# Performance work log

Hardware: AMD Instinct MI355X
Metric: run time of the kernel (lower is better)

## Reference

```python
import jax, jax.numpy as jnp
import numpy as np

T, B, I, H = 512, 64, 512, 512

def setup_inputs() -> dict:
    key = jax.random.key(0)
    k1, k2, k3 = jax.random.split(key, 3)
    # scale weights to keep tanh out of deep saturation
    return {
        "input": jax.random.normal(k1, (T, B, I), dtype=jnp.float32),
        "w_ih": jax.random.normal(k2, (H, I), dtype=jnp.float32) / np.sqrt(I),
        "w_hh": jax.random.normal(k3, (H, H), dtype=jnp.float32) / np.sqrt(H),
    }

def reference(input, w_ih, w_hh):
    # vanilla tanh RNN: h_t = tanh(x_t @ w_ih^T + h_{t-1} @ w_hh^T)
    batch = input.shape[1]
    h0 = jnp.zeros((batch, w_hh.shape[0]), dtype=input.dtype)

    def step(h_prev, x):
        h = jnp.tanh(x @ w_ih.T + h_prev @ w_hh.T)
        return h, h

    h_last, h_all = jax.lax.scan(step, h0, input)
    return h_all, h_last
```

## Files before the change

### kernel.cpp

```cpp
#include <hip/hip_runtime.h>
#include <cmath>

#define T_STEPS 512
#define BATCH   64
#define ISZ     512
#define HSZ     512
#define EXN     32768

__device__ __forceinline__ void ex_store(unsigned long long* w, float h, unsigned tag) {
    union { float f; unsigned u; } c; c.f = h;
    const unsigned long long v = ((unsigned long long)tag << 32) | (unsigned long long)c.u;
    __hip_atomic_store(w, v, __ATOMIC_RELAXED, __HIP_MEMORY_SCOPE_AGENT);
}

__device__ __forceinline__ float4 ld_pin_f4(const float* p) {
    float4 v;
    asm volatile("global_load_dwordx4 %0, %1, off" : "=v"(v) : "v"(p));
    return v;
}

__device__ __forceinline__ float dot16_fold(const float4 (&W)[4][4],
                                            const float4* __restrict__ src,
                                            int parbase4, int kseg) {
    const float4* s0 = src + parbase4 + kseg * 5;
    const float4* s1 = s0 + 160;
    float A0 = 0.f, A1 = 0.f, A2 = 0.f, A3 = 0.f;
    float B0 = 0.f, B1 = 0.f, B2 = 0.f, B3 = 0.f;
    #pragma unroll
    for (int i = 0; i < 4; ++i) {
        const float4 h0 = s0[i];
        const float4 h1 = s1[i];
        const float4 w0 = W[0][i], w1 = W[1][i], w2 = W[2][i], w3 = W[3][i];
        A0 = fmaf(w0.x, h0.x, A0); A0 = fmaf(w0.y, h0.y, A0);
        A0 = fmaf(w0.z, h0.z, A0); A0 = fmaf(w0.w, h0.w, A0);
        A1 = fmaf(w1.x, h0.x, A1); A1 = fmaf(w1.y, h0.y, A1);
        A1 = fmaf(w1.z, h0.z, A1); A1 = fmaf(w1.w, h0.w, A1);
        A2 = fmaf(w2.x, h0.x, A2); A2 = fmaf(w2.y, h0.y, A2);
        A2 = fmaf(w2.z, h0.z, A2); A2 = fmaf(w2.w, h0.w, A2);
        A3 = fmaf(w3.x, h0.x, A3); A3 = fmaf(w3.y, h0.y, A3);
        A3 = fmaf(w3.z, h0.z, A3); A3 = fmaf(w3.w, h0.w, A3);
        B0 = fmaf(w0.x, h1.x, B0); B0 = fmaf(w0.y, h1.y, B0);
        B0 = fmaf(w0.z, h1.z, B0); B0 = fmaf(w0.w, h1.w, B0);
        B1 = fmaf(w1.x, h1.x, B1); B1 = fmaf(w1.y, h1.y, B1);
        B1 = fmaf(w1.z, h1.z, B1); B1 = fmaf(w1.w, h1.w, B1);
        B2 = fmaf(w2.x, h1.x, B2); B2 = fmaf(w2.y, h1.y, B2);
        B2 = fmaf(w2.z, h1.z, B2); B2 = fmaf(w2.w, h1.w, B2);
        B3 = fmaf(w3.x, h1.x, B3); B3 = fmaf(w3.y, h1.y, B3);
        B3 = fmaf(w3.z, h1.z, B3); B3 = fmaf(w3.w, h1.w, B3);
    }
    const bool sb0 = (kseg & 1) != 0;
    const bool sb1 = (kseg & 2) != 0;
    const bool sb2 = (kseg & 4) != 0;
    const float u0 = (sb0 ? B0 : A0) + __shfl_xor(sb0 ? A0 : B0, 1, 64);
    const float u1 = (sb0 ? B1 : A1) + __shfl_xor(sb0 ? A1 : B1, 1, 64);
    const float u2 = (sb0 ? B2 : A2) + __shfl_xor(sb0 ? A2 : B2, 1, 64);
    const float u3 = (sb0 ? B3 : A3) + __shfl_xor(sb0 ? A3 : B3, 1, 64);
    const float w01 = (sb1 ? u1 : u0) + __shfl_xor(sb1 ? u0 : u1, 2, 64);
    const float w23 = (sb1 ? u3 : u2) + __shfl_xor(sb1 ? u2 : u3, 2, 64);
    float z = (sb2 ? w23 : w01) + __shfl_xor(sb2 ? w01 : w23, 4, 64);
    z += __shfl_xor(z, 8, 64);
    z += __shfl_xor(z, 16, 64);
    return z;
}

__global__ __launch_bounds__(512, 2) void rnn_fused(const float* __restrict__ x,
                                                    const float* __restrict__ wih,
                                                    const float* __restrict__ whh,
                                                    float* __restrict__ out,
                                                    unsigned long long* __restrict__ ex) {
    __shared__ __align__(16) float hls[2560];
    __shared__ __align__(16) float xss[2560];
    const float4* hl4 = (const float4*)hls;
    const float4* xs4 = (const float4*)xss;

    const int tid  = threadIdx.x;
    const int bid  = blockIdx.x;
    const int xcd  = bid & 7;
    const int ib   = bid >> 3;
    const int p    = xcd * 4 + (ib & 3);
    const int g    = ib >> 2;
    const int kseg = tid & 31;
    const int jg   = tid >> 5;
    const int jb   = g * 64 + jg * 4;

    float4 wh[4][4], wi[4][4];
    #pragma unroll
    for (int r = 0; r < 4; ++r) {
        const float* hr = whh + (size_t)(jb + r) * HSZ + kseg * 16;
        const float* ir = wih + (size_t)(jb + r) * ISZ + kseg * 16;
        #pragma unroll
        for (int i = 0; i < 4; ++i) {
            wh[r][i] = ld_pin_f4(hr + 4 * i);
            wi[r][i] = ld_pin_f4(ir + 4 * i);
        }
    }
    asm volatile("s_waitcnt vmcnt(0)" ::: "memory");
    __builtin_amdgcn_sched_barrier(0);

    unsigned long long* exw0 = ex + (size_t)(2 * p + 0) * 512 + tid;
    unsigned long long* exw1 = ex + (size_t)(2 * p + 1) * 512 + tid;

    const int whf = (tid >> 4) * 20 + ((tid >> 2) & 3) * 4 + (tid & 3);

    const int bx = tid >> 8;
    const int io = (tid & 255) * 2;
    const int xf = bx * 640 + (io >> 4) * 20 + ((io >> 2) & 3) * 4 + (io & 3);
    const float* xsrc = x + (size_t)(2 * p + bx) * ISZ + io;

    const int row  = ((kseg >> 1) & 1) + 2 * ((kseg >> 2) & 1);
    const int br   = kseg & 1;
    const int outj = jb + row;
    const int outb = 2 * p + br;
    float* outp = out + (size_t)outb * HSZ + outj;
    unsigned long long* exself = ex + (size_t)outb * 512 + outj;

    {
        const float2 v = *(const float2*)xsrc;
        *(float2*)&xss[xf] = v;
    }
    __syncthreads();
    float xwv = dot16_fold(wi, xs4, 0, kseg);

    for (int t = 0; t < T_STEPS; ++t) {
        const int  parh4 = (t & 1) * 320;
        const bool havex = (t < T_STEPS - 1);

        float2 xv;
        if (havex) xv = *(const float2*)(xsrc + (size_t)(t + 1) * (BATCH * ISZ));

        if (t > 0) {
            const size_t soff = (size_t)((t - 1) & 1) * EXN;
            unsigned long long v0 = __hip_atomic_load(exw0 + soff, __ATOMIC_RELAXED,
                                                      __HIP_MEMORY_SCOPE_AGENT);
            unsigned long long v1 = __hip_atomic_load(exw1 + soff, __ATOMIC_RELAXED,
                                                      __HIP_MEMORY_SCOPE_AGENT);
            while ((unsigned)(v0 >> 32) != (unsigned)t ||
                   (unsigned)(v1 >> 32) != (unsigned)t) {
                __builtin_amdgcn_s_sleep(1);
                v0 = __hip_atomic_load(exw0 + soff, __ATOMIC_RELAXED,
                                       __HIP_MEMORY_SCOPE_AGENT);
                v1 = __hip_atomic_load(exw1 + soff, __ATOMIC_RELAXED,
                                       __HIP_MEMORY_SCOPE_AGENT);
            }
            union { unsigned u; float f; } c0, c1;
            c0.u = (unsigned)v0; c1.u = (unsigned)v1;
            hls[parh4 * 4 + whf]       = c0.f;
            hls[parh4 * 4 + 640 + whf] = c1.f;
        }
        if (havex) *(float2*)&xss[((t + 1) & 1) * 1280 + xf] = xv;
        __syncthreads();

        float acc = 0.f;
        if (t > 0)
            acc = dot16_fold(wh, hl4, parh4, kseg);

        if (kseg < 8) {
            const float a2 = acc + xwv;
            const float e  = __expf(2.f * a2);
            const float hv = 1.f - 2.f / (e + 1.f);
            outp[(size_t)t * (BATCH * HSZ)] = hv;
            if (havex)
                ex_store(exself + (size_t)(t & 1) * EXN, hv, (unsigned)(t + 1));
            else
                out[(size_t)T_STEPS * BATCH * HSZ + (size_t)outb * HSZ + outj] = hv;
        }

        if (havex)
            xwv = dot16_fold(wi, xs4, ((t + 1) & 1) * 320, kseg);
    }
}

extern "C" void kernel_launch(void* const* d_in, const int* in_sizes, int n_in,
                              void* d_out, int out_size, void* d_ws, size_t ws_size,
                              hipStream_t stream) {
    (void)in_sizes; (void)n_in; (void)out_size; (void)ws_size;
    const float* x   = (const float*)d_in[0];
    const float* wih = (const float*)d_in[1];
    const float* whh = (const float*)d_in[2];
    float*       out = (float*)d_out;
    unsigned long long* ex = (unsigned long long*)d_ws;

    (void)hipMemsetAsync(d_ws, 0, 2 * EXN * sizeof(unsigned long long), stream);

    hipLaunchKernelGGL(rnn_fused, dim3(256), dim3(512), 0, stream,
                       x, wih, whh, out, ex);
}
```

Baseline: 1.020 ms.

## Split batch work into two pipelined halves with 2-row weight tiles per thread

Each block now owns 4 batch rows and 32 hidden units instead of 2 batch rows and 64 units, with each thread holding 2 weight rows rather than 4, which halves register-resident weights. Each timestep is split into two phases. The block waits on the exchange flags for the first batch pair, computes and publishes those results, then waits on the second pair. This lets other blocks' dependencies on the first pair resolve earlier and shortens the per-thread dot product, at the cost of an extra __syncthreads, more flag polling per step, and single-buffered LDS reuse that relies on the barrier ordering.

After: 1.916 ms. 87.7% more time.

```diff
diff --git a/kernel.cpp b/kernel.cpp
--- a/kernel.cpp
+++ b/kernel.cpp
@@ -19,45 +19,32 @@
     return v;
 }
 
-__device__ __forceinline__ float dot16_fold(const float4 (&W)[4][4],
-                                            const float4* __restrict__ src,
-                                            int parbase4, int kseg) {
-    const float4* s0 = src + parbase4 + kseg * 5;
+__device__ __forceinline__ float dot2_fold(const float4 (&W)[2][4],
+                                           const float4* __restrict__ src,
+                                           int base4, int kseg) {
+    const float4* s0 = src + base4 + kseg * 5;
     const float4* s1 = s0 + 160;
-    float A0 = 0.f, A1 = 0.f, A2 = 0.f, A3 = 0.f;
-    float B0 = 0.f, B1 = 0.f, B2 = 0.f, B3 = 0.f;
+    float A0 = 0.f, A1 = 0.f, B0 = 0.f, B1 = 0.f;
     #pragma unroll
     for (int i = 0; i < 4; ++i) {
         const float4 h0 = s0[i];
         const float4 h1 = s1[i];
-        const float4 w0 = W[0][i], w1 = W[1][i], w2 = W[2][i], w3 = W[3][i];
+        const float4 w0 = W[0][i], w1 = W[1][i];
         A0 = fmaf(w0.x, h0.x, A0); A0 = fmaf(w0.y, h0.y, A0);
         A0 = fmaf(w0.z, h0.z, A0); A0 = fmaf(w0.w, h0.w, A0);
         A1 = fmaf(w1.x, h0.x, A1); A1 = fmaf(w1.y, h0.y, A1);
         A1 = fmaf(w1.z, h0.z, A1); A1 = fmaf(w1.w, h0.w, A1);
-        A2 = fmaf(w2.x, h0.x, A2); A2 = fmaf(w2.y, h0.y, A2);
-        A2 = fmaf(w2.z, h0.z, A2); A2 = fmaf(w2.w, h0.w, A2);
-        A3 = fmaf(w3.x, h0.x, A3); A3 = fmaf(w3.y, h0.y, A3);
-        A3 = fmaf(w3.z, h0.z, A3); A3 = fmaf(w3.w, h0.w, A3);
         B0 = fmaf(w0.x, h1.x, B0); B0 = fmaf(w0.y, h1.y, B0);
         B0 = fmaf(w0.z, h1.z, B0); B0 = fmaf(w0.w, h1.w, B0);
         B1 = fmaf(w1.x, h1.x, B1); B1 = fmaf(w1.y, h1.y, B1);
         B1 = fmaf(w1.z, h1.z, B1); B1 = fmaf(w1.w, h1.w, B1);
-        B2 = fmaf(w2.x, h1.x, B2); B2 = fmaf(w2.y, h1.y, B2);
-        B2 = fmaf(w2.z, h1.z, B2); B2 = fmaf(w2.w, h1.w, B2);
-        B3 = fmaf(w3.x, h1.x, B3); B3 = fmaf(w3.y, h1.y, B3);
-        B3 = fmaf(w3.z, h1.z, B3); B3 = fmaf(w3.w, h1.w, B3);
     }
     const bool sb0 = (kseg & 1) != 0;
     const bool sb1 = (kseg & 2) != 0;
-    const bool sb2 = (kseg & 4) != 0;
     const float u0 = (sb0 ? B0 : A0) + __shfl_xor(sb0 ? A0 : B0, 1, 64);
     const float u1 = (sb0 ? B1 : A1) + __shfl_xor(sb0 ? A1 : B1, 1, 64);
-    const float u2 = (sb0 ? B2 : A2) + __shfl_xor(sb0 ? A2 : B2, 1, 64);
-    const float u3 = (sb0 ? B3 : A3) + __shfl_xor(sb0 ? A3 : B3, 1, 64);
-    const float w01 = (sb1 ? u1 : u0) + __shfl_xor(sb1 ? u0 : u1, 2, 64);
-    const float w23 = (sb1 ? u3 : u2) + __shfl_xor(sb1 ? u2 : u3, 2, 64);
-    float z = (sb2 ? w23 : w01) + __shfl_xor(sb2 ? w01 : w23, 4, 64);
+    float z = (sb1 ? u1 : u0) + __shfl_xor(sb1 ? u0 : u1, 2, 64);
+    z += __shfl_xor(z, 4, 64);
     z += __shfl_xor(z, 8, 64);
     z += __shfl_xor(z, 16, 64);
     return z;
@@ -77,15 +64,16 @@
     const int bid  = blockIdx.x;
     const int xcd  = bid & 7;
     const int ib   = bid >> 3;
-    const int p    = xcd * 4 + (ib & 3);
-    const int g    = ib >> 2;
+    const int pg   = xcd * 2 + (ib & 1);
+    const int g    = ib >> 1;
     const int kseg = tid & 31;
     const int jg   = tid >> 5;
-    const int jb   = g * 64 + jg * 4;
-
-    float4 wh[4][4], wi[4][4];
+    const int jb   = g * 32 + jg * 2;
+    const int b0   = pg * 4;
+
+    float4 wh[2][4], wi[2][4];
     #pragma unroll
-    for (int r = 0; r < 4; ++r) {
+    for (int r = 0; r < 2; ++r) {
         const float* hr = whh + (size_t)(jb + r) * HSZ + kseg * 16;
         const float* ir = wih + (size_t)(jb + r) * ISZ + kseg * 16;
         #pragma unroll
@@ -97,76 +85,116 @@
     asm volatile("s_waitcnt vmcnt(0)" ::: "memory");
     __builtin_amdgcn_sched_barrier(0);
 
-    unsigned long long* exw0 = ex + (size_t)(2 * p + 0) * 512 + tid;
-    unsigned long long* exw1 = ex + (size_t)(2 * p + 1) * 512 + tid;
+    unsigned long long* exw00 = ex + (size_t)(b0 + 0) * 512 + tid;
+    unsigned long long* exw01 = ex + (size_t)(b0 + 1) * 512 + tid;
+    unsigned long long* exw10 = ex + (size_t)(b0 + 2) * 512 + tid;
+    unsigned long long* exw11 = ex + (size_t)(b0 + 3) * 512 + tid;
 
     const int whf = (tid >> 4) * 20 + ((tid >> 2) & 3) * 4 + (tid & 3);
 
-    const int bx = tid >> 8;
-    const int io = (tid & 255) * 2;
-    const int xf = bx * 640 + (io >> 4) * 20 + ((io >> 2) & 3) * 4 + (io & 3);
-    const float* xsrc = x + (size_t)(2 * p + bx) * ISZ + io;
-
-    const int row  = ((kseg >> 1) & 1) + 2 * ((kseg >> 2) & 1);
-    const int br   = kseg & 1;
+    const int bx  = tid >> 7;
+    const int idx = tid & 127;
+    const int xf4 = bx * 160 + (idx >> 2) * 5 + (idx & 3);
+    const float* xsrc = x + (size_t)(b0 + bx) * ISZ + idx * 4;
+
+    const int bsel = kseg & 1;
+    const int row  = (kseg >> 1) & 1;
     const int outj = jb + row;
-    const int outb = 2 * p + br;
-    float* outp = out + (size_t)outb * HSZ + outj;
-    unsigned long long* exself = ex + (size_t)outb * 512 + outj;
-
-    {
-        const float2 v = *(const float2*)xsrc;
-        *(float2*)&xss[xf] = v;
-    }
+    const int ob0  = b0 + bsel;
+    const int ob1  = b0 + 2 + bsel;
+    float* outp0 = out + (size_t)ob0 * HSZ + outj;
+    float* outp1 = out + (size_t)ob1 * HSZ + outj;
+    unsigned long long* exs0 = ex + (size_t)ob0 * 512 + outj;
+    unsigned long long* exs1 = ex + (size_t)ob1 * 512 + outj;
+
+    ((float4*)xss)[xf4] = *(const float4*)xsrc;
     __syncthreads();
-    float xwv = dot16_fold(wi, xs4, 0, kseg);
+    float xw0 = dot2_fold(wi, xs4, 0,   kseg);
+    float xw1 = dot2_fold(wi, xs4, 320, kseg);
 
     for (int t = 0; t < T_STEPS; ++t) {
-        const int  parh4 = (t & 1) * 320;
         const bool havex = (t < T_STEPS - 1);
 
-        float2 xv;
-        if (havex) xv = *(const float2*)(xsrc + (size_t)(t + 1) * (BATCH * ISZ));
+        float4 xv;
+        if (havex) xv = *(const float4*)(xsrc + (size_t)(t + 1) * (BATCH * ISZ));
+
+        const size_t soff = (size_t)((t - 1) & 1) * EXN;
 
         if (t > 0) {
-            const size_t soff = (size_t)((t - 1) & 1) * EXN;
-            unsigned long long v0 = __hip_atomic_load(exw0 + soff, __ATOMIC_RELAXED,
-                                                      __HIP_MEMORY_SCOPE_AGENT);
-            unsigned long long v1 = __hip_atomic_load(exw1 + soff, __ATOMIC_RELAXED,
+            unsigned long long v0 = __hip_atomic_load(exw00 + soff, __ATOMIC_RELAXED,
+                                                      __HIP_MEMORY_SCOPE_AGENT);
+            unsigned long long v1 = __hip_atomic_load(exw01 + soff, __ATOMIC_RELAXED,
                                                       __HIP_MEMORY_SCOPE_AGENT);
             while ((unsigned)(v0 >> 32) != (unsigned)t ||
                    (unsigned)(v1 >> 32) != (unsigned)t) {
                 __builtin_amdgcn_s_sleep(1);
-                v0 = __hip_atomic_load(exw0 + soff, __ATOMIC_RELAXED,
-                                       __HIP_MEMORY_SCOPE_AGENT);
-                v1 = __hip_atomic_load(exw1 + soff, __ATOMIC_RELAXED,
+                v0 = __hip_atomic_load(exw00 + soff, __ATOMIC_RELAXED,
+                                       __HIP_MEMORY_SCOPE_AGENT);
+                v1 = __hip_atomic_load(exw01 + soff, __ATOMIC_RELAXED,
                                        __HIP_MEMORY_SCOPE_AGENT);
             }
             union { unsigned u; float f; } c0, c1;
             c0.u = (unsigned)v0; c1.u = (unsigned)v1;
-            hls[parh4 * 4 + whf]       = c0.f;
-            hls[parh4 * 4 + 640 + whf] = c1.f;
-        }
-        if (havex) *(float2*)&xss[((t + 1) & 1) * 1280 + xf] = xv;
+            hls[whf]       = c0.f;
+            hls[640 + whf] = c1.f;
+        }
         __syncthreads();
 
-        float acc = 0.f;
-        if (t > 0)
-            acc = dot16_fold(wh, hl4, parh4, kseg);
-
-        if (kseg < 8) {
-            const float a2 = acc + xwv;
-            const float e  = __expf(2.f * a2);
-            const float hv = 1.f - 2.f / (e + 1.f);
-            outp[(size_t)t * (BATCH * HSZ)] = hv;
-            if (havex)
-                ex_store(exself + (size_t)(t & 1) * EXN, hv, (unsigned)(t + 1));
-            else
-                out[(size_t)T_STEPS * BATCH * HSZ + (size_t)outb * HSZ + outj] = hv;
-        }
-
-        if (havex)
-            xwv = dot16_fold(wi, xs4, ((t + 1) & 1) * 320, kseg);
+        {
+            float acc = 0.f;
+            if (t > 0) acc = dot2_fold(wh, hl4, 0, kseg);
+            if (kseg < 4) {
+                const float a2 = acc + xw0;
+                const float e  = __expf(2.f * a2);
+                const float hv = 1.f - 2.f / (e + 1.f);
+                outp0[(size_t)t * (BATCH * HSZ)] = hv;
+                if (havex)
+                    ex_store(exs0 + (size_t)(t & 1) * EXN, hv, (unsigned)(t + 1));
+                else
+                    out[(size_t)T_STEPS * BATCH * HSZ + (size_t)ob0 * HSZ + outj] = hv;
+            }
+        }
+
+        if (t > 0) {
+            unsigned long long v0 = __hip_atomic_load(exw10 + soff, __ATOMIC_RELAXED,
+                                                      __HIP_MEMORY_SCOPE_AGENT);
+            unsigned long long v1 = __hip_atomic_load(exw11 + soff, __ATOMIC_RELAXED,
+                                                      __HIP_MEMORY_SCOPE_AGENT);
+            while ((unsigned)(v0 >> 32) != (unsigned)t ||
+                   (unsigned)(v1 >> 32) != (unsigned)t) {
+                __builtin_amdgcn_s_sleep(1);
+                v0 = __hip_atomic_load(exw10 + soff, __ATOMIC_RELAXED,
+                                       __HIP_MEMORY_SCOPE_AGENT);
+                v1 = __hip_atomic_load(exw11 + soff, __ATOMIC_RELAXED,
+                                       __HIP_MEMORY_SCOPE_AGENT);
+            }
+            union { unsigned u; float f; } c0, c1;
+            c0.u = (unsigned)v0; c1.u = (unsigned)v1;
+            hls[1280 + whf] = c0.f;
+            hls[1920 + whf] = c1.f;
+        }
+        if (havex) ((float4*)xss)[xf4] = xv;
+        __syncthreads();
+
+        {
+            float acc = 0.f;
+            if (t > 0) acc = dot2_fold(wh, hl4, 320, kseg);
+            if (kseg < 4) {
+                const float a2 = acc + xw1;
+                const float e  = __expf(2.f * a2);
+                const float hv = 1.f - 2.f / (e + 1.f);
+                outp1[(size_t)t * (BATCH * HSZ)] = hv;
+                if (havex)
+                    ex_store(exs1 + (size_t)(t & 1) * EXN, hv, (unsigned)(t + 1));
+                else
+                    out[(size_t)T_STEPS * BATCH * HSZ + (size_t)ob1 * HSZ + outj] = hv;
+            }
+        }
+
+        if (havex) {
+            xw0 = dot2_fold(wi, xs4, 0,   kseg);
+            xw1 = dot2_fold(wi, xs4, 320, kseg);
+        }
     }
 }
 
```

## Split RNN into input-projection phase then recurrence with one batch per block

Applied to the files above, without the earlier changes.

The kernel now first computes x_t·W_ih^T for all timesteps into the output buffer, with no cross-block sync. It then reloads W_hh into the same registers and runs the recurrence, reading the precomputed projection back. Each block now handles one batch row and 8 output rows per thread group instead of two batch rows and 4 rows. This halves the weight registers per thread and removes the input dot product from the serial critical path. The cost is a full extra write and read of a T×B×H intermediate through global memory, and each block still has to poll the exchange buffer every step.

New measurement: 1.165 ms. 1.14x slower.

```diff
diff --git a/kernel.cpp b/kernel.cpp
--- a/kernel.cpp
+++ b/kernel.cpp
@@ -19,45 +19,42 @@
     return v;
 }
 
-__device__ __forceinline__ float dot16_fold(const float4 (&W)[4][4],
-                                            const float4* __restrict__ src,
-                                            int parbase4, int kseg) {
-    const float4* s0 = src + parbase4 + kseg * 5;
-    const float4* s1 = s0 + 160;
-    float A0 = 0.f, A1 = 0.f, A2 = 0.f, A3 = 0.f;
-    float B0 = 0.f, B1 = 0.f, B2 = 0.f, B3 = 0.f;
+__device__ __forceinline__ float dot8_fold(const float4 (&W)[8][4],
+                                           const float4* __restrict__ src,
+                                           int base4, int kseg) {
+    const float4* s = src + base4 + kseg * 5;
+    float a0 = 0.f, a1 = 0.f, a2 = 0.f, a3 = 0.f;
+    float a4 = 0.f, a5 = 0.f, a6 = 0.f, a7 = 0.f;
     #pragma unroll
     for (int i = 0; i < 4; ++i) {
-        const float4 h0 = s0[i];
-        const float4 h1 = s1[i];
-        const float4 w0 = W[0][i], w1 = W[1][i], w2 = W[2][i], w3 = W[3][i];
-        A0 = fmaf(w0.x, h0.x, A0); A0 = fmaf(w0.y, h0.y, A0);
-        A0 = fmaf(w0.z, h0.z, A0); A0 = fmaf(w0.w, h0.w, A0);
-        A1 = fmaf(w1.x, h0.x, A1); A1 = fmaf(w1.y, h0.y, A1);
-        A1 = fmaf(w1.z, h0.z, A1); A1 = fmaf(w1.w, h0.w, A1);
-        A2 = fmaf(w2.x, h0.x, A2); A2 = fmaf(w2.y, h0.y, A2);
-        A2 = fmaf(w2.z, h0.z, A2); A2 = fmaf(w2.w, h0.w, A2);
-        A3 = fmaf(w3.x, h0.x, A3); A3 = fmaf(w3.y, h0.y, A3);
-        A3 = fmaf(w3.z, h0.z, A3); A3 = fmaf(w3.w, h0.w, A3);
-        B0 = fmaf(w0.x, h1.x, B0); B0 = fmaf(w0.y, h1.y, B0);
-        B0 = fmaf(w0.z, h1.z, B0); B0 = fmaf(w0.w, h1.w, B0);
-        B1 = fmaf(w1.x, h1.x, B1); B1 = fmaf(w1.y, h1.y, B1);
-        B1 = fmaf(w1.z, h1.z, B1); B1 = fmaf(w1.w, h1.w, B1);
-        B2 = fmaf(w2.x, h1.x, B2); B2 = fmaf(w2.y, h1.y, B2);
-        B2 = fmaf(w2.z, h1.z, B2); B2 = fmaf(w2.w, h1.w, B2);
-        B3 = fmaf(w3.x, h1.x, B3); B3 = fmaf(w3.y, h1.y, B3);
-        B3 = fmaf(w3.z, h1.z, B3); B3 = fmaf(w3.w, h1.w, B3);
+        const float4 h = s[i];
+        a0 = fmaf(W[0][i].x, h.x, a0); a0 = fmaf(W[0][i].y, h.y, a0);
+        a0 = fmaf(W[0][i].z, h.z, a0); a0 = fmaf(W[0][i].w, h.w, a0);
+        a1 = fmaf(W[1][i].x, h.x, a1); a1 = fmaf(W[1][i].y, h.y, a1);
+        a1 = fmaf(W[1][i].z, h.z, a1); a1 = fmaf(W[1][i].w, h.w, a1);
+        a2 = fmaf(W[2][i].x, h.x, a2); a2 = fmaf(W[2][i].y, h.y, a2);
+        a2 = fmaf(W[2][i].z, h.z, a2); a2 = fmaf(W[2][i].w, h.w, a2);
+        a3 = fmaf(W[3][i].x, h.x, a3); a3 = fmaf(W[3][i].y, h.y, a3);
+        a3 = fmaf(W[3][i].z, h.z, a3); a3 = fmaf(W[3][i].w, h.w, a3);
+        a4 = fmaf(W[4][i].x, h.x, a4); a4 = fmaf(W[4][i].y, h.y, a4);
+        a4 = fmaf(W[4][i].z, h.z, a4); a4 = fmaf(W[4][i].w, h.w, a4);
+        a5 = fmaf(W[5][i].x, h.x, a5); a5 = fmaf(W[5][i].y, h.y, a5);
+        a5 = fmaf(W[5][i].z, h.z, a5); a5 = fmaf(W[5][i].w, h.w, a5);
+        a6 = fmaf(W[6][i].x, h.x, a6); a6 = fmaf(W[6][i].y, h.y, a6);
+        a6 = fmaf(W[6][i].z, h.z, a6); a6 = fmaf(W[6][i].w, h.w, a6);
+        a7 = fmaf(W[7][i].x, h.x, a7); a7 = fmaf(W[7][i].y, h.y, a7);
+        a7 = fmaf(W[7][i].z, h.z, a7); a7 = fmaf(W[7][i].w, h.w, a7);
     }
     const bool sb0 = (kseg & 1) != 0;
     const bool sb1 = (kseg & 2) != 0;
     const bool sb2 = (kseg & 4) != 0;
-    const float u0 = (sb0 ? B0 : A0) + __shfl_xor(sb0 ? A0 : B0, 1, 64);
-    const float u1 = (sb0 ? B1 : A1) + __shfl_xor(sb0 ? A1 : B1, 1, 64);
-    const float u2 = (sb0 ? B2 : A2) + __shfl_xor(sb0 ? A2 : B2, 1, 64);
-    const float u3 = (sb0 ? B3 : A3) + __shfl_xor(sb0 ? A3 : B3, 1, 64);
-    const float w01 = (sb1 ? u1 : u0) + __shfl_xor(sb1 ? u0 : u1, 2, 64);
-    const float w23 = (sb1 ? u3 : u2) + __shfl_xor(sb1 ? u2 : u3, 2, 64);
-    float z = (sb2 ? w23 : w01) + __shfl_xor(sb2 ? w01 : w23, 4, 64);
+    const float u0 = (sb0 ? a1 : a0) + __shfl_xor(sb0 ? a0 : a1, 1, 64);
+    const float u1 = (sb0 ? a3 : a2) + __shfl_xor(sb0 ? a2 : a3, 1, 64);
+    const float u2 = (sb0 ? a5 : a4) + __shfl_xor(sb0 ? a4 : a5, 1, 64);
+    const float u3 = (sb0 ? a7 : a6) + __shfl_xor(sb0 ? a6 : a7, 1, 64);
+    const float v0 = (sb1 ? u1 : u0) + __shfl_xor(sb1 ? u0 : u1, 2, 64);
+    const float v1 = (sb1 ? u3 : u2) + __shfl_xor(sb1 ? u2 : u3, 2, 64);
+    float z = (sb2 ? v1 : v0) + __shfl_xor(sb2 ? v0 : v1, 4, 64);
     z += __shfl_xor(z, 8, 64);
     z += __shfl_xor(z, 16, 64);
     return z;
@@ -68,91 +65,87 @@
                                                     const float* __restrict__ whh,
                                                     float* __restrict__ out,
                                                     unsigned long long* __restrict__ ex) {
-    __shared__ __align__(16) float hls[2560];
-    __shared__ __align__(16) float xss[2560];
-    const float4* hl4 = (const float4*)hls;
-    const float4* xs4 = (const float4*)xss;
+    __shared__ __align__(16) float st[1280];
+    const float4* st4 = (const float4*)st;
 
     const int tid  = threadIdx.x;
     const int bid  = blockIdx.x;
     const int xcd  = bid & 7;
     const int ib   = bid >> 3;
-    const int p    = xcd * 4 + (ib & 3);
-    const int g    = ib >> 2;
+    const int b    = xcd * 8 + (ib & 7);
+    const int g    = ib >> 3;
     const int kseg = tid & 31;
     const int jg   = tid >> 5;
-    const int jb   = g * 64 + jg * 4;
+    const int jb   = g * 128 + jg * 8;
 
-    float4 wh[4][4], wi[4][4];
+    const int whf = (tid >> 4) * 20 + ((tid >> 2) & 3) * 4 + (tid & 3);
+
+    const float* xcol = x + (size_t)b * ISZ + tid;
+
+    const int outj = jb + (kseg & 7);
+    float* outp = out + (size_t)b * HSZ + outj;
+    unsigned long long* exw    = ex + (size_t)b * 512 + tid;
+    unsigned long long* exself = ex + (size_t)b * 512 + outj;
+
+    float4 w[8][4];
     #pragma unroll
-    for (int r = 0; r < 4; ++r) {
-        const float* hr = whh + (size_t)(jb + r) * HSZ + kseg * 16;
+    for (int r = 0; r < 8; ++r) {
         const float* ir = wih + (size_t)(jb + r) * ISZ + kseg * 16;
         #pragma unroll
-        for (int i = 0; i < 4; ++i) {
-            wh[r][i] = ld_pin_f4(hr + 4 * i);
-            wi[r][i] = ld_pin_f4(ir + 4 * i);
-        }
+        for (int i = 0; i < 4; ++i)
+            w[r][i] = ld_pin_f4(ir + 4 * i);
     }
     asm volatile("s_waitcnt vmcnt(0)" ::: "memory");
     __builtin_amdgcn_sched_barrier(0);
 
-    unsigned long long* exw0 = ex + (size_t)(2 * p + 0) * 512 + tid;
-    unsigned long long* exw1 = ex + (size_t)(2 * p + 1) * 512 + tid;
+    st[whf] = xcol[0];
+    __syncthreads();
+    for (int t = 0; t < T_STEPS; ++t) {
+        float xv = 0.f;
+        if (t < T_STEPS - 1) xv = xcol[(size_t)(t + 1) * (BATCH * ISZ)];
+        const float v = dot8_fold(w, st4, (t & 1) * 160, kseg);
+        if (kseg < 8) outp[(size_t)t * (BATCH * HSZ)] = v;
+        if (t < T_STEPS - 1) st[((t + 1) & 1) * 640 + whf] = xv;
+        __syncthreads();
+    }
 
-    const int whf = (tid >> 4) * 20 + ((tid >> 2) & 3) * 4 + (tid & 3);
+    asm volatile("" ::: "memory");
+    #pragma unroll
+    for (int r = 0; r < 8; ++r) {
+        const float* hr = whh + (size_t)(jb + r) * HSZ + kseg * 16;
+        #pragma unroll
+        for (int i = 0; i < 4; ++i)
+            w[r][i] = ld_pin_f4(hr + 4 * i);
+    }
+    asm volatile("s_waitcnt vmcnt(0)" ::: "memory");
+    __builtin_amdgcn_sched_barrier(0);
+    __syncthreads();
 
-    const int bx = tid >> 8;
-    const int io = (tid & 255) * 2;
-    const int xf = bx * 640 + (io >> 4) * 20 + ((io >> 2) & 3) * 4 + (io & 3);
-    const float* xsrc = x + (size_t)(2 * p + bx) * ISZ + io;
-
-    const int row  = ((kseg >> 1) & 1) + 2 * ((kseg >> 2) & 1);
-    const int br   = kseg & 1;
-    const int outj = jb + row;
-    const int outb = 2 * p + br;
-    float* outp = out + (size_t)outb * HSZ + outj;
-    unsigned long long* exself = ex + (size_t)outb * 512 + outj;
-
-    {
-        const float2 v = *(const float2*)xsrc;
-        *(float2*)&xss[xf] = v;
-    }
-    __syncthreads();
-    float xwv = dot16_fold(wi, xs4, 0, kseg);
+    float xwv = outp[0];
 
     for (int t = 0; t < T_STEPS; ++t) {
-        const int  parh4 = (t & 1) * 320;
         const bool havex = (t < T_STEPS - 1);
 
-        float2 xv;
-        if (havex) xv = *(const float2*)(xsrc + (size_t)(t + 1) * (BATCH * ISZ));
+        float xwn = 0.f;
+        if (havex) xwn = outp[(size_t)(t + 1) * (BATCH * HSZ)];
 
         if (t > 0) {
             const size_t soff = (size_t)((t - 1) & 1) * EXN;
-            unsigned long long v0 = __hip_atomic_load(exw0 + soff, __ATOMIC_RELAXED,
-                                                      __HIP_MEMORY_SCOPE_AGENT);
-            unsigned long long v1 = __hip_atomic_load(exw1 + soff, __ATOMIC_RELAXED,
-                                                      __HIP_MEMORY_SCOPE_AGENT);
-            while ((unsigned)(v0 >> 32) != (unsigned)t ||
-                   (unsigned)(v1 >> 32) != (unsigned)t) {
+            unsigned long long v = __hip_atomic_load(exw + soff, __ATOMIC_RELAXED,
+                                                     __HIP_MEMORY_SCOPE_AGENT);
+            while ((unsigned)(v >> 32) != (unsigned)t) {
                 __builtin_amdgcn_s_sleep(1);
-                v0 = __hip_atomic_load(exw0 + soff, __ATOMIC_RELAXED,
-                                       __HIP_MEMORY_SCOPE_AGENT);
-                v1 = __hip_atomic_load(exw1 + soff, __ATOMIC_RELAXED,
-                                       __HIP_MEMORY_SCOPE_AGENT);
+                v = __hip_atomic_load(exw + soff, __ATOMIC_RELAXED,
+                                      __HIP_MEMORY_SCOPE_AGENT);
             }
-            union { unsigned u; float f; } c0, c1;
-            c0.u = (unsigned)v0; c1.u = (unsigned)v1;
-            hls[parh4 * 4 + whf]       = c0.f;
-            hls[parh4 * 4 + 640 + whf] = c1.f;
+            union { unsigned u; float f; } c; c.u = (unsigned)v;
+            st[(t & 1) * 640 + whf] = c.f;
         }
-        if (havex) *(float2*)&xss[((t + 1) & 1) * 1280 + xf] = xv;
         __syncthreads();
 
         float acc = 0.f;
         if (t > 0)
-            acc = dot16_fold(wh, hl4, parh4, kseg);
+            acc = dot8_fold(w, st4, (t & 1) * 160, kseg);
 
         if (kseg < 8) {
             const float a2 = acc + xwv;
@@ -162,11 +155,9 @@
             if (havex)
                 ex_store(exself + (size_t)(t & 1) * EXN, hv, (unsigned)(t + 1));
             else
-                out[(size_t)T_STEPS * BATCH * HSZ + (size_t)outb * HSZ + outj] = hv;
+                out[(size_t)T_STEPS * BATCH * HSZ + (size_t)b * HSZ + outj] = hv;
         }
-
-        if (havex)
-            xwv = dot16_fold(wi, xs4, ((t + 1) & 1) * 320, kseg);
+        xwv = xwn;
     }
 }
 
```

## Split each step into two per-batch-row phases to overlap exchange waits with compute

Applied to the files above, without the earlier changes.

Each block's two batch rows are now processed one at a time. The block waits only for row 0's hidden state, computes and publishes row 0, then waits for row 1, so work on the first row overlaps with the global exchange latency of the second. The fused 16-way dot product becomes two 4-way dot products with a simpler shuffle reduction. The cost is an extra __syncthreads per step, and only 4 of every 32 lanes write in each phase, which adds serialization.

Result: slower. 1.418 ms (+38.9%).

```diff
diff --git a/kernel.cpp b/kernel.cpp
--- a/kernel.cpp
+++ b/kernel.cpp
@@ -19,45 +19,30 @@
     return v;
 }
 
-__device__ __forceinline__ float dot16_fold(const float4 (&W)[4][4],
-                                            const float4* __restrict__ src,
-                                            int parbase4, int kseg) {
-    const float4* s0 = src + parbase4 + kseg * 5;
-    const float4* s1 = s0 + 160;
-    float A0 = 0.f, A1 = 0.f, A2 = 0.f, A3 = 0.f;
-    float B0 = 0.f, B1 = 0.f, B2 = 0.f, B3 = 0.f;
+__device__ __forceinline__ float dot4_fold(const float4 (&W)[4][4],
+                                           const float4* __restrict__ src,
+                                           int base4, int kseg) {
+    const float4* s = src + base4 + kseg * 5;
+    float a0 = 0.f, a1 = 0.f, a2 = 0.f, a3 = 0.f;
     #pragma unroll
     for (int i = 0; i < 4; ++i) {
-        const float4 h0 = s0[i];
-        const float4 h1 = s1[i];
+        const float4 h = s[i];
         const float4 w0 = W[0][i], w1 = W[1][i], w2 = W[2][i], w3 = W[3][i];
-        A0 = fmaf(w0.x, h0.x, A0); A0 = fmaf(w0.y, h0.y, A0);
-        A0 = fmaf(w0.z, h0.z, A0); A0 = fmaf(w0.w, h0.w, A0);
-        A1 = fmaf(w1.x, h0.x, A1); A1 = fmaf(w1.y, h0.y, A1);
-        A1 = fmaf(w1.z, h0.z, A1); A1 = fmaf(w1.w, h0.w, A1);
-        A2 = fmaf(w2.x, h0.x, A2); A2 = fmaf(w2.y, h0.y, A2);
-        A2 = fmaf(w2.z, h0.z, A2); A2 = fmaf(w2.w, h0.w, A2);
-        A3 = fmaf(w3.x, h0.x, A3); A3 = fmaf(w3.y, h0.y, A3);
-        A3 = fmaf(w3.z, h0.z, A3); A3 = fmaf(w3.w, h0.w, A3);
-        B0 = fmaf(w0.x, h1.x, B0); B0 = fmaf(w0.y, h1.y, B0);
-        B0 = fmaf(w0.z, h1.z, B0); B0 = fmaf(w0.w, h1.w, B0);
-        B1 = fmaf(w1.x, h1.x, B1); B1 = fmaf(w1.y, h1.y, B1);
-        B1 = fmaf(w1.z, h1.z, B1); B1 = fmaf(w1.w, h1.w, B1);
-        B2 = fmaf(w2.x, h1.x, B2); B2 = fmaf(w2.y, h1.y, B2);
-        B2 = fmaf(w2.z, h1.z, B2); B2 = fmaf(w2.w, h1.w, B2);
-        B3 = fmaf(w3.x, h1.x, B3); B3 = fmaf(w3.y, h1.y, B3);
-        B3 = fmaf(w3.z, h1.z, B3); B3 = fmaf(w3.w, h1.w, B3);
+        a0 = fmaf(w0.x, h.x, a0); a0 = fmaf(w0.y, h.y, a0);
+        a0 = fmaf(w0.z, h.z, a0); a0 = fmaf(w0.w, h.w, a0);
+        a1 = fmaf(w1.x, h.x, a1); a1 = fmaf(w1.y, h.y, a1);
+        a1 = fmaf(w1.z, h.z, a1); a1 = fmaf(w1.w, h.w, a1);
+        a2 = fmaf(w2.x, h.x, a2); a2 = fmaf(w2.y, h.y, a2);
+        a2 = fmaf(w2.z, h.z, a2); a2 = fmaf(w2.w, h.w, a2);
+        a3 = fmaf(w3.x, h.x, a3); a3 = fmaf(w3.y, h.y, a3);
+        a3 = fmaf(w3.z, h.z, a3); a3 = fmaf(w3.w, h.w, a3);
     }
     const bool sb0 = (kseg & 1) != 0;
     const bool sb1 = (kseg & 2) != 0;
-    const bool sb2 = (kseg & 4) != 0;
-    const float u0 = (sb0 ? B0 : A0) + __shfl_xor(sb0 ? A0 : B0, 1, 64);
-    const float u1 = (sb0 ? B1 : A1) + __shfl_xor(sb0 ? A1 : B1, 1, 64);
-    const float u2 = (sb0 ? B2 : A2) + __shfl_xor(sb0 ? A2 : B2, 1, 64);
-    const float u3 = (sb0 ? B3 : A3) + __shfl_xor(sb0 ? A3 : B3, 1, 64);
-    const float w01 = (sb1 ? u1 : u0) + __shfl_xor(sb1 ? u0 : u1, 2, 64);
-    const float w23 = (sb1 ? u3 : u2) + __shfl_xor(sb1 ? u2 : u3, 2, 64);
-    float z = (sb2 ? w23 : w01) + __shfl_xor(sb2 ? w01 : w23, 4, 64);
+    const float u0 = (sb0 ? a1 : a0) + __shfl_xor(sb0 ? a0 : a1, 1, 64);
+    const float u1 = (sb0 ? a3 : a2) + __shfl_xor(sb0 ? a2 : a3, 1, 64);
+    float z = (sb1 ? u1 : u0) + __shfl_xor(sb1 ? u0 : u1, 2, 64);
+    z += __shfl_xor(z, 4, 64);
     z += __shfl_xor(z, 8, 64);
     z += __shfl_xor(z, 16, 64);
     return z;
@@ -107,66 +92,88 @@
     const int xf = bx * 640 + (io >> 4) * 20 + ((io >> 2) & 3) * 4 + (io & 3);
     const float* xsrc = x + (size_t)(2 * p + bx) * ISZ + io;
 
-    const int row  = ((kseg >> 1) & 1) + 2 * ((kseg >> 2) & 1);
-    const int br   = kseg & 1;
-    const int outj = jb + row;
-    const int outb = 2 * p + br;
-    float* outp = out + (size_t)outb * HSZ + outj;
-    unsigned long long* exself = ex + (size_t)outb * 512 + outj;
+    const int outj = jb + (kseg & 3);
+    const int ob0  = 2 * p;
+    const int ob1  = 2 * p + 1;
+    float* outp0 = out + (size_t)ob0 * HSZ + outj;
+    float* outp1 = out + (size_t)ob1 * HSZ + outj;
+    unsigned long long* exs0 = ex + (size_t)ob0 * 512 + outj;
+    unsigned long long* exs1 = ex + (size_t)ob1 * 512 + outj;
 
     {
         const float2 v = *(const float2*)xsrc;
         *(float2*)&xss[xf] = v;
     }
     __syncthreads();
-    float xwv = dot16_fold(wi, xs4, 0, kseg);
+    float xw0 = dot4_fold(wi, xs4, 0,   kseg);
+    float xw1 = dot4_fold(wi, xs4, 160, kseg);
 
     for (int t = 0; t < T_STEPS; ++t) {
         const int  parh4 = (t & 1) * 320;
         const bool havex = (t < T_STEPS - 1);
+        const size_t soff = (size_t)((t - 1) & 1) * EXN;
 
         float2 xv;
         if (havex) xv = *(const float2*)(xsrc + (size_t)(t + 1) * (BATCH * ISZ));
 
         if (t > 0) {
-            const size_t soff = (size_t)((t - 1) & 1) * EXN;
-            unsigned long long v0 = __hip_atomic_load(exw0 + soff, __ATOMIC_RELAXED,
-                                                      __HIP_MEMORY_SCOPE_AGENT);
-            unsigned long long v1 = __hip_atomic_load(exw1 + soff, __ATOMIC_RELAXED,
-                                                      __HIP_MEMORY_SCOPE_AGENT);
-            while ((unsigned)(v0 >> 32) != (unsigned)t ||
-                   (unsigned)(v1 >> 32) != (unsigned)t) {
+            unsigned long long v = __hip_atomic_load(exw0 + soff, __ATOMIC_RELAXED,
+                                                     __HIP_MEMORY_SCOPE_AGENT);
+            while ((unsigned)(v >> 32) != (unsigned)t) {
                 __builtin_amdgcn_s_sleep(1);
-                v0 = __hip_atomic_load(exw0 + soff, __ATOMIC_RELAXED,
-                                       __HIP_MEMORY_SCOPE_AGENT);
-                v1 = __hip_atomic_load(exw1 + soff, __ATOMIC_RELAXED,
-                                       __HIP_MEMORY_SCOPE_AGENT);
+                v = __hip_atomic_load(exw0 + soff, __ATOMIC_RELAXED,
+                                      __HIP_MEMORY_SCOPE_AGENT);
             }
-            union { unsigned u; float f; } c0, c1;
-            c0.u = (unsigned)v0; c1.u = (unsigned)v1;
-            hls[parh4 * 4 + whf]       = c0.f;
-            hls[parh4 * 4 + 640 + whf] = c1.f;
+            union { unsigned u; float f; } c; c.u = (unsigned)v;
+            hls[parh4 * 4 + whf] = c.f;
         }
         if (havex) *(float2*)&xss[((t + 1) & 1) * 1280 + xf] = xv;
         __syncthreads();
 
-        float acc = 0.f;
-        if (t > 0)
-            acc = dot16_fold(wh, hl4, parh4, kseg);
+        {
+            float acc = 0.f;
+            if (t > 0) acc = dot4_fold(wh, hl4, parh4, kseg);
+            if (kseg < 4) {
+                const float a2 = acc + xw0;
+                const float e  = __expf(2.f * a2);
+                const float hv = 1.f - 2.f / (e + 1.f);
+                outp0[(size_t)t * (BATCH * HSZ)] = hv;
+                if (havex)
+                    ex_store(exs0 + (size_t)(t & 1) * EXN, hv, (unsigned)(t + 1));
+                else
+                    out[(size_t)T_STEPS * BATCH * HSZ + (size_t)ob0 * HSZ + outj] = hv;
+            }
+        }
+        if (havex) xw0 = dot4_fold(wi, xs4, ((t + 1) & 1) * 320, kseg);
 
-        if (kseg < 8) {
-            const float a2 = acc + xwv;
-            const float e  = __expf(2.f * a2);
-            const float hv = 1.f - 2.f / (e + 1.f);
-            outp[(size_t)t * (BATCH * HSZ)] = hv;
-            if (havex)
-                ex_store(exself + (size_t)(t & 1) * EXN, hv, (unsigned)(t + 1));
-            else
-                out[(size_t)T_STEPS * BATCH * HSZ + (size_t)outb * HSZ + outj] = hv;
+        if (t > 0) {
+            unsigned long long v = __hip_atomic_load(exw1 + soff, __ATOMIC_RELAXED,
+                                                     __HIP_MEMORY_SCOPE_AGENT);
+            while ((unsigned)(v >> 32) != (unsigned)t) {
+                __builtin_amdgcn_s_sleep(1);
+                v = __hip_atomic_load(exw1 + soff, __ATOMIC_RELAXED,
+                                      __HIP_MEMORY_SCOPE_AGENT);
+            }
+            union { unsigned u; float f; } c; c.u = (unsigned)v;
+            hls[parh4 * 4 + 640 + whf] = c.f;
         }
+        __syncthreads();
 
-        if (havex)
-            xwv = dot16_fold(wi, xs4, ((t + 1) & 1) * 320, kseg);
+        {
+            float acc = 0.f;
+            if (t > 0) acc = dot4_fold(wh, hl4, parh4 + 160, kseg);
+            if (kseg < 4) {
+                const float a2 = acc + xw1;
+                const float e  = __expf(2.f * a2);
+                const float hv = 1.f - 2.f / (e + 1.f);
+                outp1[(size_t)t * (BATCH * HSZ)] = hv;
+                if (havex)
+                    ex_store(exs1 + (size_t)(t & 1) * EXN, hv, (unsigned)(t + 1));
+                else
+                    out[(size_t)T_STEPS * BATCH * HSZ + (size_t)ob1 * HSZ + outj] = hv;
+            }
+        }
+        if (havex) xw1 = dot4_fold(wi, xs4, ((t + 1) & 1) * 320 + 160, kseg);
     }
 }
 
```
